# Performance work log

Measured on AMD Instinct MI355X. Metric: run time of the kernel, lower is better.

## Reference

```python
import jax, jax.numpy as jnp
import numpy as np

B, S, D, H = 4, 2048, 1024, 16
Dh = D // H


def _layernorm(x, a, b):
    # torch.var default is unbiased (ddof=1)
    mu = jnp.mean(x, axis=-1, keepdims=True)
    sg = jnp.var(x, axis=-1, keepdims=True, ddof=1)
    return (x - mu) / jnp.sqrt(sg + 1e-08) * a + b


def setup_inputs() -> dict:
    key = jax.random.key(0)
    ks = jax.random.split(key, 16)
    s = 1.0 / np.sqrt(D)
    inp = {
        'q': jax.random.normal(ks[0], (B, S, D), jnp.float32),
        'k': jax.random.normal(ks[1], (B, S, D), jnp.float32),
        'v': jax.random.normal(ks[2], (B, S, D), jnp.float32),
        'g': jax.random.normal(ks[3], (B, S, D), jnp.float32),
        # causal mask: True = masked
        'm': jnp.triu(jnp.ones((S, S), jnp.bool_), k=1)[None, None],
        'Wq': jax.random.uniform(ks[4], (D, D), jnp.float32, -s, s),
        'bq': jnp.zeros((D,), jnp.float32),
        'Wk': jax.random.uniform(ks[5], (D, D), jnp.float32, -s, s),
        'bk': jnp.zeros((D,), jnp.float32),
        'Wv': jax.random.uniform(ks[6], (D, D), jnp.float32, -s, s),
        'bv': jnp.zeros((D,), jnp.float32),
        'Wg': jax.random.uniform(ks[7], (D, D), jnp.float32, -s, s),
        'bg': jnp.zeros((D,), jnp.float32),
        'ln_a': jnp.ones((D,), jnp.float32),
        'ln_b': jnp.zeros((D,), jnp.float32),
        'Wo': jax.random.uniform(ks[8], (D, D), jnp.float32, -s, s),
        'bo': jnp.zeros((D,), jnp.float32),
    }
    return inp


def reference(q, k, v, g, m, Wq, bq, Wk, bk, Wv, bv, Wg, bg, ln_a, ln_b, Wo, bo):
    qp = q @ Wq.T + bq
    kp = k @ Wk.T + bk
    vp = v @ Wv.T + bv
    gp = g @ Wg.T + bg
    # gating path: exact GELU (torch default), then custom LayerNorm (unbiased var)
    vp = jax.nn.gelu(vp, approximate=False)
    gp = jax.nn.gelu(gp, approximate=False)
    vp = _layernorm(vp, ln_a, ln_b)
    # [B,S,D] -> [B,H,S,Dh]
    qh = qp.reshape(B, S, H, Dh).transpose(0, 2, 1, 3)
    kh = kp.reshape(B, S, H, Dh).transpose(0, 2, 1, 3)
    vh = vp.reshape(B, S, H, Dh).transpose(0, 2, 1, 3)
    gh = gp.reshape(B, S, H, Dh).transpose(0, 2, 1, 3)
    a = jnp.einsum('bhqd,bhkd->bhqk', qh, kh) / jnp.sqrt(jnp.float32(Dh))
    a = jnp.where(m, -jnp.inf, a)
    a = jax.nn.softmax(a, axis=-1)
    # dropout = 0.0 (inference): no-op
    o = jnp.einsum('bhqk,bhkd->bhqd', a, vh)
    o = o * gh
    o = o.transpose(0, 2, 1, 3).reshape(B, S, D)
    o = o @ Wo.T + bo
    return (o, a)
```

## Files before the change

### kernel.cpp

```cpp
#include <hip/hip_runtime.h>
#include <hip/hip_bf16.h>
#include <cstdint>
#include <cstddef>

#define DEVINL static __device__ __forceinline__

typedef short bf16x8 __attribute__((ext_vector_type(8)));
typedef float f32x4  __attribute__((ext_vector_type(4)));
typedef unsigned short u16;

static constexpr int Bb = 4, Ss = 2048, Dd = 1024, Hh = 16, DhC = 64;
static constexpr int Mrows = Bb * Ss;
static constexpr int BHc = Bb * Hh;

DEVINL u16 f2bf(float f) {
    union { float f; uint32_t u; } v; v.f = f;
    uint32_t r = v.u + 0x7fffu + ((v.u >> 16) & 1u);
    return (u16)(r >> 16);
}
DEVINL float bf2f(u16 h) {
    union { uint32_t u; float f; } v; v.u = ((uint32_t)h) << 16;
    return v.f;
}
DEVINL float gelu_exact(float x) {
    return 0.5f * x * (1.0f + erff(x * 0.70710678118654752f));
}
DEVINL void gload16(const u16* gsrc, u16* ldsdst) {
    auto* g = reinterpret_cast<const __attribute__((address_space(1))) uint32_t*>(
        reinterpret_cast<uintptr_t>(gsrc));
    auto* l = reinterpret_cast<__attribute__((address_space(3))) uint32_t*>(
        reinterpret_cast<uintptr_t>(ldsdst));
    __builtin_amdgcn_global_load_lds(g, l, 16, 0, 0);
}

__global__ __launch_bounds__(256) void k_cvt_bf16(const float* __restrict__ src,
                                                  u16* __restrict__ dst, int n4) {
    int i = blockIdx.x * 256 + threadIdx.x;
    if (i >= n4) return;
    float4 v = ((const float4*)src)[i];
    ushort4 o;
    o.x = f2bf(v.x); o.y = f2bf(v.y); o.z = f2bf(v.z); o.w = f2bf(v.w);
    ((ushort4*)dst)[i] = o;
}

template<int EPI, bool ABF16>
__global__ __launch_bounds__(256) void k_gemm_bt(
    const void* __restrict__ Ap, const u16* __restrict__ Wp,
    const float* __restrict__ bias, void* __restrict__ Cp,
    int Msz, int Nsz, int Ksz)
{
    __shared__ u16 As[128 * 32];
    __shared__ u16 Bs[128 * 32];
    const int tid = threadIdx.x, lane = tid & 63, w = tid >> 6;
    const int wm = w >> 1, wn = w & 1;
    const int m0 = blockIdx.y * 128, n0 = blockIdx.x * 128;
    const int g = lane >> 4, li = lane & 15;

    const f32x4 zero4 = {0.f, 0.f, 0.f, 0.f};
    f32x4 acc[4][4];
#pragma unroll
    for (int m = 0; m < 4; m++)
#pragma unroll
        for (int n = 0; n < 4; n++) acc[m][n] = zero4;

    for (int k0 = 0; k0 < Ksz; k0 += 32) {
        __syncthreads();
        if (ABF16) {
            const u16* A = (const u16*)Ap;
#pragma unroll
            for (int i = 0; i < 2; i++) {
                int chunk = (w * 2 + i) * 64 + lane;
                int row = chunk >> 2, cp = chunk & 3;
                gload16(A + (size_t)(m0 + row) * Ksz + k0 + ((cp ^ ((row >> 1) & 3)) << 3),
                        &As[(w * 2 + i) * 512]);
            }
        } else {
            const float* A = (const float*)Ap;
#pragma unroll
            for (int i = 0; i < 4; i++) {
                int u = i * 256 + tid;
                int row = u >> 3, c4 = u & 7;
                float4 v = *(const float4*)(A + (size_t)(m0 + row) * Ksz + k0 + c4 * 4);
                ushort4 o;
                o.x = f2bf(v.x); o.y = f2bf(v.y); o.z = f2bf(v.z); o.w = f2bf(v.w);
                int off = row * 32 + ((((c4 >> 1) ^ ((row >> 1) & 3))) << 3) + ((c4 & 1) << 2);
                *(ushort4*)&As[off] = o;
            }
        }
#pragma unroll
        for (int i = 0; i < 2; i++) {
            int chunk = (w * 2 + i) * 64 + lane;
            int row = chunk >> 2, cp = chunk & 3;
            gload16(Wp + (size_t)(n0 + row) * Ksz + k0 + ((cp ^ ((row >> 1) & 3)) << 3),
                    &Bs[(w * 2 + i) * 512]);
        }
        __syncthreads();

        bf16x8 af[4], bfr[4];
#pragma unroll
        for (int m = 0; m < 4; m++) {
            int row = wm * 64 + m * 16 + li;
            af[m] = *(const bf16x8*)&As[row * 32 + ((g ^ ((row >> 1) & 3)) << 3)];
        }
#pragma unroll
        for (int n = 0; n < 4; n++) {
            int row = wn * 64 + n * 16 + li;
            bfr[n] = *(const bf16x8*)&Bs[row * 32 + ((g ^ ((row >> 1) & 3)) << 3)];
        }
#pragma unroll
        for (int m = 0; m < 4; m++)
#pragma unroll
            for (int n = 0; n < 4; n++)
                acc[m][n] = __builtin_amdgcn_mfma_f32_16x16x32_bf16(af[m], bfr[n], acc[m][n], 0, 0, 0);
    }

#pragma unroll
    for (int m = 0; m < 4; m++) {
#pragma unroll
        for (int n = 0; n < 4; n++) {
            int col = n0 + wn * 64 + n * 16 + li;
            float bv = bias[col];
#pragma unroll
            for (int r = 0; r < 4; r++) {
                int row = m0 + wm * 64 + m * 16 + g * 4 + r;
                float v = acc[m][n][r] + bv;
                if (EPI == 1 || EPI == 2) v = gelu_exact(v);
                if (EPI == 0 || EPI == 1)
                    ((u16*)Cp)[(size_t)row * Nsz + col] = f2bf(v);
                else
                    ((float*)Cp)[(size_t)row * Nsz + col] = v;
            }
        }
    }
}

__global__ __launch_bounds__(256) void k_ln(const float* __restrict__ vp,
                                            const float* __restrict__ la,
                                            const float* __restrict__ lb,
                                            u16* __restrict__ vh) {
    int row = blockIdx.x;
    const float* x = vp + (size_t)row * 1024;
    int tid = threadIdx.x;
    float4 v = ((const float4*)x)[tid];
    float s = v.x + v.y + v.z + v.w;
    float s2 = v.x * v.x + v.y * v.y + v.z * v.z + v.w * v.w;
#pragma unroll
    for (int off = 1; off < 64; off <<= 1) {
        s  += __shfl_xor(s, off, 64);
        s2 += __shfl_xor(s2, off, 64);
    }
    __shared__ float red[8];
    int w = tid >> 6, lane = tid & 63;
    if (lane == 0) { red[w] = s; red[4 + w] = s2; }
    __syncthreads();
    s  = red[0] + red[1] + red[2] + red[3];
    s2 = red[4] + red[5] + red[6] + red[7];
    float mu = s * (1.0f / 1024.0f);
    float var = (s2 - 1024.0f * mu * mu) * (1.0f / 1023.0f);
    float rs = rsqrtf(var + 1e-8f);
    float4 a4 = ((const float4*)la)[tid];
    float4 b4 = ((const float4*)lb)[tid];
    ushort4 o;
    o.x = f2bf((v.x - mu) * rs * a4.x + b4.x);
    o.y = f2bf((v.y - mu) * rs * a4.y + b4.y);
    o.z = f2bf((v.z - mu) * rs * a4.z + b4.z);
    o.w = f2bf((v.w - mu) * rs * a4.w + b4.w);
    ((ushort4*)(vh + (size_t)row * 1024))[tid] = o;
}

__global__ __launch_bounds__(256) void k_transpose(const u16* __restrict__ vh,
                                                   u16* __restrict__ vhT) {
    int bh = blockIdx.y, b = bh >> 4, h = bh & 15, s0 = blockIdx.x * 64;
    __shared__ u16 t[64 * 96];
    int tid = threadIdx.x;
#pragma unroll
    for (int j = 0; j < 2; j++) {
        int u = j * 256 + tid;
        int r = u >> 3, c8 = u & 7;
        bf16x8 v = *(const bf16x8*)(vh + ((size_t)(b * 2048 + s0 + r) * 1024 + h * 64 + c8 * 8));
        *(bf16x8*)&t[r * 96 + c8 * 8] = v;
    }
    __syncthreads();
#pragma unroll
    for (int j = 0; j < 2; j++) {
        int u = j * 256 + tid;
        int d = u >> 3, s8 = u & 7;
        bf16x8 vv;
#pragma unroll
        for (int jj = 0; jj < 8; jj++) vv[jj] = (short)t[(s8 * 8 + jj) * 96 + d];
        *(bf16x8*)(vhT + ((size_t)(bh * 64 + d) * 2048 + s0 + s8 * 8)) = vv;
    }
}

__global__ __launch_bounds__(256) void k_attn_stats(const u16* __restrict__ qp,
                                                    const u16* __restrict__ kp,
                                                    float2* __restrict__ ml) {
    __shared__ u16 Ks[128 * 64];
    const int tid = threadIdx.x, lane = tid & 63, w = tid >> 6;
    const int g = lane >> 4, li = lane & 15;
    const int bh = blockIdx.y, b = bh >> 4, h = bh & 15;
    const int q0 = blockIdx.x * 64;
    const int qrow = q0 + w * 16 + li;
    const u16* qbase = qp + ((size_t)(b * 2048 + qrow) * 1024 + h * 64 + g * 8);
    bf16x8 qa0 = *(const bf16x8*)qbase;
    bf16x8 qa1 = *(const bf16x8*)(qbase + 32);
    float m_run[4] = {-1e30f, -1e30f, -1e30f, -1e30f};
    float l_run[4] = {0.f, 0.f, 0.f, 0.f};
    const int ktmax = (q0 + 63) >> 7;
    const u16* kbh = kp + ((size_t)(b * 2048) * 1024 + h * 64);
    const f32x4 zero4 = {0.f, 0.f, 0.f, 0.f};

    for (int kt = 0; kt <= ktmax; ++kt) {
        const int k0 = kt * 128;
        __syncthreads();
#pragma unroll
        for (int i = 0; i < 4; i++) {
            int chunk = (w * 4 + i) * 64 + lane;
            int r = chunk >> 3, cp = chunk & 7;
            gload16(kbh + (size_t)(k0 + r) * 1024 + ((cp ^ (r & 7)) << 3), &Ks[(w * 4 + i) * 512]);
        }
        __syncthreads();
        f32x4 sc[8];
#pragma unroll
        for (int n = 0; n < 8; n++) {
            int rb = n * 16 + li;
            const u16* kr = &Ks[rb * 64];
            bf16x8 kb0 = *(const bf16x8*)&kr[(g ^ (rb & 7)) << 3];
            bf16x8 kb1 = *(const bf16x8*)&kr[((g + 4) ^ (rb & 7)) << 3];
            f32x4 c = zero4;
            c = __builtin_amdgcn_mfma_f32_16x16x32_bf16(qa0, kb0, c, 0, 0, 0);
            c = __builtin_amdgcn_mfma_f32_16x16x32_bf16(qa1, kb1, c, 0, 0, 0);
            sc[n] = c;
        }
        float tmax[4] = {-1e30f, -1e30f, -1e30f, -1e30f};
#pragma unroll
        for (int n = 0; n < 8; n++) {
            int col = k0 + n * 16 + li;
#pragma unroll
            for (int r = 0; r < 4; r++) {
                int rowq = q0 + w * 16 + g * 4 + r;
                float sv = (col <= rowq) ? sc[n][r] * 0.125f : -1e30f;
                sc[n][r] = sv;
                tmax[r] = fmaxf(tmax[r], sv);
            }
        }
#pragma unroll
        for (int r = 0; r < 4; r++) {
#pragma unroll
            for (int off = 1; off < 16; off <<= 1)
                tmax[r] = fmaxf(tmax[r], __shfl_xor(tmax[r], off, 64));
            float mn = fmaxf(m_run[r], tmax[r]);
            float ts = 0.f;
#pragma unroll
            for (int n = 0; n < 8; n++) ts += __expf(sc[n][r] - mn);
#pragma unroll
            for (int off = 1; off < 16; off <<= 1)
                ts += __shfl_xor(ts, off, 64);
            l_run[r] = l_run[r] * __expf(m_run[r] - mn) + ts;
            m_run[r] = mn;
        }
    }
    if (li == 0) {
#pragma unroll
        for (int r = 0; r < 4; r++) {
            int rowq = q0 + w * 16 + g * 4 + r;
            ml[(size_t)bh * 2048 + rowq] = make_float2(m_run[r], l_run[r]);
        }
    }
}

__global__ __launch_bounds__(256) void k_attn_pv(const u16* __restrict__ qp,
                                                 const u16* __restrict__ kp,
                                                 const u16* __restrict__ vhT,
                                                 const u16* __restrict__ gh,
                                                 const float2* __restrict__ ml,
                                                 float* __restrict__ aout,
                                                 u16* __restrict__ gated) {
    __shared__ u16 Ks[128 * 64];
    __shared__ u16 Vs[64 * 128];
    __shared__ u16 Ps[4 * 16 * 128];
    const int tid = threadIdx.x, lane = tid & 63, w = tid >> 6;
    const int g = lane >> 4, li = lane & 15;
    const int bh = blockIdx.y, b = bh >> 4, h = bh & 15;
    const int q0 = blockIdx.x * 64;
    const int qrow0 = q0 + w * 16;
    const u16* qbase = qp + ((size_t)(b * 2048 + qrow0 + li) * 1024 + h * 64 + g * 8);
    bf16x8 qa0 = *(const bf16x8*)qbase;
    bf16x8 qa1 = *(const bf16x8*)(qbase + 32);
    float m_row[4], linv[4];
#pragma unroll
    for (int r = 0; r < 4; r++) {
        float2 v = ml[(size_t)bh * 2048 + qrow0 + g * 4 + r];
        m_row[r] = v.x; linv[r] = 1.0f / v.y;
    }
    const f32x4 zero4 = {0.f, 0.f, 0.f, 0.f};
    f32x4 oacc[4];
#pragma unroll
    for (int n = 0; n < 4; n++) oacc[n] = zero4;
    const int ktmax = (q0 + 63) >> 7;
    float* arow = aout + (size_t)bh * 2048 * 2048;
    const u16* kbh = kp + ((size_t)(b * 2048) * 1024 + h * 64);
    const u16* vbh = vhT + (size_t)bh * 64 * 2048;

    for (int kt = ktmax + 1; kt < 16; ++kt) {
        int k0 = kt * 128;
        float4 z = {0.f, 0.f, 0.f, 0.f};
#pragma unroll
        for (int i = 0; i < 8; i++) {
            int u = i * 64 + lane;
            *(float4*)(arow + (size_t)(qrow0 + (u >> 5)) * 2048 + k0 + (u & 31) * 4) = z;
        }
    }

    for (int kt = 0; kt <= ktmax; ++kt) {
        const int k0 = kt * 128;
        __syncthreads();
#pragma unroll
        for (int i = 0; i < 4; i++) {
            int chunk = (w * 4 + i) * 64 + lane;
            int r = chunk >> 3, cp = chunk & 7;
            gload16(kbh + (size_t)(k0 + r) * 1024 + ((cp ^ (r & 7)) << 3), &Ks[(w * 4 + i) * 512]);
        }
#pragma unroll
        for (int i = 0; i < 4; i++) {
            int chunk = (w * 4 + i) * 64 + lane;
            int r = chunk >> 4, cp = chunk & 15;
            gload16(vbh + (size_t)r * 2048 + k0 + ((cp ^ (r & 7)) << 3), &Vs[(w * 4 + i) * 512]);
        }
        __syncthreads();
        f32x4 sc[8];
#pragma unroll
        for (int n = 0; n < 8; n++) {
            int rb = n * 16 + li;
            const u16* kr = &Ks[rb * 64];
            bf16x8 kb0 = *(const bf16x8*)&kr[(g ^ (rb & 7)) << 3];
            bf16x8 kb1 = *(const bf16x8*)&kr[((g + 4) ^ (rb & 7)) << 3];
            f32x4 c = zero4;
            c = __builtin_amdgcn_mfma_f32_16x16x32_bf16(qa0, kb0, c, 0, 0, 0);
            c = __builtin_amdgcn_mfma_f32_16x16x32_bf16(qa1, kb1, c, 0, 0, 0);
            sc[n] = c;
        }
#pragma unroll
        for (int n = 0; n < 8; n++) {
            int col = k0 + n * 16 + li;
#pragma unroll
            for (int r = 0; r < 4; r++) {
                int rowq = qrow0 + g * 4 + r;
                float p = (col <= rowq) ? __expf(sc[n][r] * 0.125f - m_row[r]) * linv[r] : 0.0f;
                sc[n][r] = p;
                arow[(size_t)rowq * 2048 + col] = p;
            }
        }
        u16* Pw = &Ps[w * 2048];
#pragma unroll
        for (int n = 0; n < 8; n++) {
            int colb = n * 16 + li;
            int c = colb >> 3, wi = colb & 7;
#pragma unroll
            for (int r = 0; r < 4; r++) {
                int lr = g * 4 + r;
                Pw[lr * 128 + ((c ^ (lr & 7)) << 3) + wi] = f2bf(sc[n][r]);
            }
        }
#pragma unroll
        for (int ks = 0; ks < 4; ++ks) {
            int cl = ks * 4 + g;
            bf16x8 pa = *(const bf16x8*)&Pw[li * 128 + ((cl ^ (li & 7)) << 3)];
#pragma unroll
            for (int n = 0; n < 4; n++) {
                int vr = n * 16 + li;
                bf16x8 vb = *(const bf16x8*)&Vs[vr * 128 + ((cl ^ (vr & 7)) << 3)];
                oacc[n] = __builtin_amdgcn_mfma_f32_16x16x32_bf16(pa, vb, oacc[n], 0, 0, 0);
            }
        }
    }
    const u16* ghb_base = gh + (size_t)(b * 2048) * 1024 + h * 64;
#pragma unroll
    for (int n = 0; n < 4; n++) {
#pragma unroll
        for (int r = 0; r < 4; r++) {
            int rowq = qrow0 + g * 4 + r;
            int d = n * 16 + li;
            float gv = bf2f(ghb_base[(size_t)rowq * 1024 + d]);
            gated[((size_t)(b * 2048 + rowq)) * 1024 + h * 64 + d] = f2bf(oacc[n][r] * gv);
        }
    }
}

extern "C" void kernel_launch(void* const* d_in, const int* in_sizes, int n_in,
                              void* d_out, int out_size, void* d_ws, size_t ws_size,
                              hipStream_t stream) {
    const float* q  = (const float*)d_in[0];
    const float* k  = (const float*)d_in[1];
    const float* v  = (const float*)d_in[2];
    const float* g  = (const float*)d_in[3];
    const float* Wq = (const float*)d_in[5];
    const float* bq = (const float*)d_in[6];
    const float* Wk = (const float*)d_in[7];
    const float* bk = (const float*)d_in[8];
    const float* Wv = (const float*)d_in[9];
    const float* bv = (const float*)d_in[10];
    const float* Wg = (const float*)d_in[11];
    const float* bg = (const float*)d_in[12];
    const float* ln_a = (const float*)d_in[13];
    const float* ln_b = (const float*)d_in[14];
    const float* Wo = (const float*)d_in[15];
    const float* bo = (const float*)d_in[16];

    float* o_out = (float*)d_out;
    float* a_out = o_out + (size_t)Mrows * Dd;

    u16* qp    = (u16*)d_ws;
    u16* kpb   = qp    + (size_t)Mrows * Dd;
    u16* vhT   = kpb   + (size_t)Mrows * Dd;
    u16* ghb   = vhT   + (size_t)Mrows * Dd;
    u16* gated = ghb   + (size_t)Mrows * Dd;
    u16* Wo_bf = gated + (size_t)Mrows * Dd;
    float2* ml = (float2*)(Wo_bf + (size_t)Dd * Dd);

    u16* Wq_bf = (u16*)a_out;
    u16* Wk_bf = Wq_bf + (size_t)Dd * Dd;
    u16* Wv_bf = Wk_bf + (size_t)Dd * Dd;
    u16* Wg_bf = Wv_bf + (size_t)Dd * Dd;
    float* vp  = (float*)(Wg_bf + (size_t)Dd * Dd);
    u16* vh    = (u16*)(vp + (size_t)Mrows * Dd);

    const int n4 = Dd * Dd / 4;
    const int cb = (n4 + 255) / 256;
    k_cvt_bf16<<<cb, 256, 0, stream>>>(Wq, Wq_bf, n4);
    k_cvt_bf16<<<cb, 256, 0, stream>>>(Wk, Wk_bf, n4);
    k_cvt_bf16<<<cb, 256, 0, stream>>>(Wv, Wv_bf, n4);
    k_cvt_bf16<<<cb, 256, 0, stream>>>(Wg, Wg_bf, n4);
    k_cvt_bf16<<<cb, 256, 0, stream>>>(Wo, Wo_bf, n4);

    dim3 gg(Dd / 128, Mrows / 128);
    k_gemm_bt<0, false><<<gg, 256, 0, stream>>>(q, Wq_bf, bq, qp,  Mrows, Dd, Dd);
    k_gemm_bt<0, false><<<gg, 256, 0, stream>>>(k, Wk_bf, bk, kpb, Mrows, Dd, Dd);
    k_gemm_bt<2, false><<<gg, 256, 0, stream>>>(v, Wv_bf, bv, vp,  Mrows, Dd, Dd);
    k_gemm_bt<1, false><<<gg, 256, 0, stream>>>(g, Wg_bf, bg, ghb, Mrows, Dd, Dd);

    k_ln<<<Mrows, 256, 0, stream>>>(vp, ln_a, ln_b, vh);

    dim3 gt(Ss / 64, BHc);
    k_transpose<<<gt, 256, 0, stream>>>(vh, vhT);

    dim3 ga(Ss / 64, BHc);
    k_attn_stats<<<ga, 256, 0, stream>>>(qp, kpb, ml);
    k_attn_pv<<<ga, 256, 0, stream>>>(qp, kpb, vhT, ghb, ml, a_out, gated);

    k_gemm_bt<3, true><<<gg, 256, 0, stream>>>(gated, Wo_bf, bo, o_out, Mrows, Dd, Dd);
}
```

Before: 746.2 us.

## Transpose QK MFMA operands so each lane owns a query row

Swaps the MFMA operand order in both attention kernels so the score tile is transposed: each lane now holds four consecutive key columns for a single query row. This lets the stats kernel reduce with only two cross-lane shuffles on one scalar. It also lets the PV kernel write the attention-probability output as 16-byte f32x4 stores and pack P into LDS with 8-byte stores. The gated epilogue now stages O through LDS as bf16 and does vectorized 16-byte gate loads and output stores. The cost is an extra bf16 rounding of O before the gate multiply, plus some added LDS traffic.

```diff
diff --git a/kernel.cpp b/kernel.cpp
--- a/kernel.cpp
+++ b/kernel.cpp
@@ -6,6 +6,7 @@
 #define DEVINL static __device__ __forceinline__
 
 typedef short bf16x8 __attribute__((ext_vector_type(8)));
+typedef short s16x4  __attribute__((ext_vector_type(4)));
 typedef float f32x4  __attribute__((ext_vector_type(4)));
 typedef unsigned short u16;
 
@@ -204,8 +205,7 @@
     const u16* qbase = qp + ((size_t)(b * 2048 + qrow) * 1024 + h * 64 + g * 8);
     bf16x8 qa0 = *(const bf16x8*)qbase;
     bf16x8 qa1 = *(const bf16x8*)(qbase + 32);
-    float m_run[4] = {-1e30f, -1e30f, -1e30f, -1e30f};
-    float l_run[4] = {0.f, 0.f, 0.f, 0.f};
+    float m_run = -1e30f, l_run = 0.f;
     const int ktmax = (q0 + 63) >> 7;
     const u16* kbh = kp + ((size_t)(b * 2048) * 1024 + h * 64);
     const f32x4 zero4 = {0.f, 0.f, 0.f, 0.f};
@@ -228,45 +228,35 @@
             bf16x8 kb0 = *(const bf16x8*)&kr[(g ^ (rb & 7)) << 3];
             bf16x8 kb1 = *(const bf16x8*)&kr[((g + 4) ^ (rb & 7)) << 3];
             f32x4 c = zero4;
-            c = __builtin_amdgcn_mfma_f32_16x16x32_bf16(qa0, kb0, c, 0, 0, 0);
-            c = __builtin_amdgcn_mfma_f32_16x16x32_bf16(qa1, kb1, c, 0, 0, 0);
+            c = __builtin_amdgcn_mfma_f32_16x16x32_bf16(kb0, qa0, c, 0, 0, 0);
+            c = __builtin_amdgcn_mfma_f32_16x16x32_bf16(kb1, qa1, c, 0, 0, 0);
             sc[n] = c;
         }
-        float tmax[4] = {-1e30f, -1e30f, -1e30f, -1e30f};
+        float tmax = -1e30f;
 #pragma unroll
         for (int n = 0; n < 8; n++) {
-            int col = k0 + n * 16 + li;
 #pragma unroll
             for (int r = 0; r < 4; r++) {
-                int rowq = q0 + w * 16 + g * 4 + r;
-                float sv = (col <= rowq) ? sc[n][r] * 0.125f : -1e30f;
+                int col = k0 + n * 16 + g * 4 + r;
+                float sv = (col <= qrow) ? sc[n][r] * 0.125f : -1e30f;
                 sc[n][r] = sv;
-                tmax[r] = fmaxf(tmax[r], sv);
-            }
-        }
-#pragma unroll
-        for (int r = 0; r < 4; r++) {
-#pragma unroll
-            for (int off = 1; off < 16; off <<= 1)
-                tmax[r] = fmaxf(tmax[r], __shfl_xor(tmax[r], off, 64));
-            float mn = fmaxf(m_run[r], tmax[r]);
-            float ts = 0.f;
-#pragma unroll
-            for (int n = 0; n < 8; n++) ts += __expf(sc[n][r] - mn);
-#pragma unroll
-            for (int off = 1; off < 16; off <<= 1)
-                ts += __shfl_xor(ts, off, 64);
-            l_run[r] = l_run[r] * __expf(m_run[r] - mn) + ts;
-            m_run[r] = mn;
-        }
-    }
-    if (li == 0) {
-#pragma unroll
-        for (int r = 0; r < 4; r++) {
-            int rowq = q0 + w * 16 + g * 4 + r;
-            ml[(size_t)bh * 2048 + rowq] = make_float2(m_run[r], l_run[r]);
-        }
-    }
+                tmax = fmaxf(tmax, sv);
+            }
+        }
+        tmax = fmaxf(tmax, __shfl_xor(tmax, 16, 64));
+        tmax = fmaxf(tmax, __shfl_xor(tmax, 32, 64));
+        float mn = fmaxf(m_run, tmax);
+        float ts = 0.f;
+#pragma unroll
+        for (int n = 0; n < 8; n++)
+#pragma unroll
+            for (int r = 0; r < 4; r++) ts += __expf(sc[n][r] - mn);
+        ts += __shfl_xor(ts, 16, 64);
+        ts += __shfl_xor(ts, 32, 64);
+        l_run = l_run * __expf(m_run - mn) + ts;
+        m_run = mn;
+    }
+    if (g == 0) ml[(size_t)bh * 2048 + qrow] = make_float2(m_run, l_run);
 }
 
 __global__ __launch_bounds__(256) void k_attn_pv(const u16* __restrict__ qp,
@@ -278,21 +268,18 @@
                                                  u16* __restrict__ gated) {
     __shared__ u16 Ks[128 * 64];
     __shared__ u16 Vs[64 * 128];
-    __shared__ u16 Ps[4 * 16 * 128];
+    __shared__ short Ps[4 * 16 * 128];
     const int tid = threadIdx.x, lane = tid & 63, w = tid >> 6;
     const int g = lane >> 4, li = lane & 15;
     const int bh = blockIdx.y, b = bh >> 4, h = bh & 15;
     const int q0 = blockIdx.x * 64;
     const int qrow0 = q0 + w * 16;
-    const u16* qbase = qp + ((size_t)(b * 2048 + qrow0 + li) * 1024 + h * 64 + g * 8);
+    const int qrow = qrow0 + li;
+    const u16* qbase = qp + ((size_t)(b * 2048 + qrow) * 1024 + h * 64 + g * 8);
     bf16x8 qa0 = *(const bf16x8*)qbase;
     bf16x8 qa1 = *(const bf16x8*)(qbase + 32);
-    float m_row[4], linv[4];
-#pragma unroll
-    for (int r = 0; r < 4; r++) {
-        float2 v = ml[(size_t)bh * 2048 + qrow0 + g * 4 + r];
-        m_row[r] = v.x; linv[r] = 1.0f / v.y;
-    }
+    float2 mlv = ml[(size_t)bh * 2048 + qrow];
+    const float mrow = mlv.x, linv = 1.0f / mlv.y;
     const f32x4 zero4 = {0.f, 0.f, 0.f, 0.f};
     f32x4 oacc[4];
 #pragma unroll
@@ -312,6 +299,7 @@
         }
     }
 
+    short* Pw = &Ps[w * 2048];
     for (int kt = 0; kt <= ktmax; ++kt) {
         const int k0 = kt * 128;
         __syncthreads();
@@ -336,31 +324,24 @@
             bf16x8 kb0 = *(const bf16x8*)&kr[(g ^ (rb & 7)) << 3];
             bf16x8 kb1 = *(const bf16x8*)&kr[((g + 4) ^ (rb & 7)) << 3];
             f32x4 c = zero4;
-            c = __builtin_amdgcn_mfma_f32_16x16x32_bf16(qa0, kb0, c, 0, 0, 0);
-            c = __builtin_amdgcn_mfma_f32_16x16x32_bf16(qa1, kb1, c, 0, 0, 0);
+            c = __builtin_amdgcn_mfma_f32_16x16x32_bf16(kb0, qa0, c, 0, 0, 0);
+            c = __builtin_amdgcn_mfma_f32_16x16x32_bf16(kb1, qa1, c, 0, 0, 0);
             sc[n] = c;
         }
 #pragma unroll
         for (int n = 0; n < 8; n++) {
-            int col = k0 + n * 16 + li;
 #pragma unroll
             for (int r = 0; r < 4; r++) {
-                int rowq = qrow0 + g * 4 + r;
-                float p = (col <= rowq) ? __expf(sc[n][r] * 0.125f - m_row[r]) * linv[r] : 0.0f;
+                int col = k0 + n * 16 + g * 4 + r;
+                float p = (col <= qrow) ? __expf(sc[n][r] * 0.125f - mrow) * linv : 0.0f;
                 sc[n][r] = p;
-                arow[(size_t)rowq * 2048 + col] = p;
-            }
-        }
-        u16* Pw = &Ps[w * 2048];
-#pragma unroll
-        for (int n = 0; n < 8; n++) {
-            int colb = n * 16 + li;
-            int c = colb >> 3, wi = colb & 7;
-#pragma unroll
-            for (int r = 0; r < 4; r++) {
-                int lr = g * 4 + r;
-                Pw[lr * 128 + ((c ^ (lr & 7)) << 3) + wi] = f2bf(sc[n][r]);
-            }
+            }
+            *(f32x4*)(arow + (size_t)qrow * 2048 + k0 + n * 16 + g * 4) = sc[n];
+            s16x4 pk;
+#pragma unroll
+            for (int r = 0; r < 4; r++) pk[r] = (short)f2bf(sc[n][r]);
+            int chunk = n * 2 + (g >> 1);
+            *(s16x4*)&Pw[li * 128 + ((chunk ^ (li & 7)) << 3) + (g & 1) * 4] = pk;
         }
 #pragma unroll
         for (int ks = 0; ks < 4; ++ks) {
@@ -374,16 +355,29 @@
             }
         }
     }
+
+#pragma unroll
+    for (int n = 0; n < 4; n++) {
+        int d8 = n * 2 + (li >> 3), wi = li & 7;
+#pragma unroll
+        for (int r = 0; r < 4; r++) {
+            int lr = g * 4 + r;
+            Pw[lr * 64 + ((d8 ^ (lr & 7)) << 3) + wi] = (short)f2bf(oacc[n][r]);
+        }
+    }
     const u16* ghb_base = gh + (size_t)(b * 2048) * 1024 + h * 64;
 #pragma unroll
-    for (int n = 0; n < 4; n++) {
-#pragma unroll
-        for (int r = 0; r < 4; r++) {
-            int rowq = qrow0 + g * 4 + r;
-            int d = n * 16 + li;
-            float gv = bf2f(ghb_base[(size_t)rowq * 1024 + d]);
-            gated[((size_t)(b * 2048 + rowq)) * 1024 + h * 64 + d] = f2bf(oacc[n][r] * gv);
-        }
+    for (int it = 0; it < 2; ++it) {
+        int lr = it * 8 + (lane >> 3);
+        int c8 = lane & 7;
+        int rowq = qrow0 + lr;
+        bf16x8 ov = *(const bf16x8*)&Pw[lr * 64 + ((c8 ^ (lr & 7)) << 3)];
+        bf16x8 gv = *(const bf16x8*)(ghb_base + (size_t)rowq * 1024 + c8 * 8);
+        bf16x8 outv;
+#pragma unroll
+        for (int j = 0; j < 8; j++)
+            outv[j] = (short)f2bf(bf2f((u16)ov[j]) * bf2f((u16)gv[j]));
+        *(bf16x8*)(gated + ((size_t)(b * 2048 + rowq)) * 1024 + h * 64 + c8 * 8) = outv;
     }
 }
 
```

After: 716.9 us. 1.04x faster.
